# Kernel optimization log

Hardware: AMD Instinct MI355X
Metric: run time of the kernel (lower is better)

Reference implementation:

```python
import jax, jax.numpy as jnp
import numpy as np

# WGS84 constants
_A = 6378137.0
_E2 = 6.69437999014e-3  # first eccentricity squared

ALPHA = 1.0
GAMMA = 2.0
DYNAMIC_GAMMA = True
SCALE_FACTOR = 1.0


def _geodetic_to_ecef(lat_rad, lon_rad, h):
    sl, cl = jnp.sin(lat_rad), jnp.cos(lat_rad)
    so, co = jnp.sin(lon_rad), jnp.cos(lon_rad)
    N = _A / jnp.sqrt(1.0 - _E2 * sl * sl)
    x = (N + h) * cl * co
    y = (N + h) * cl * so
    z = (N * (1.0 - _E2) + h) * sl
    return jnp.stack([x, y, z], axis=-1)


def setup_inputs() -> dict:
    key = jax.random.key(0)
    k1, k2, k3, k4 = jax.random.split(key, 4)
    B = 4_000_000
    lat = jax.random.uniform(k1, (B,), jnp.float32, -80.0, 80.0)    # degrees
    lon = jax.random.uniform(k2, (B,), jnp.float32, -180.0, 180.0)  # degrees
    h = jax.random.uniform(k3, (B,), jnp.float32, 0.0, 1000.0)      # meters
    targets = jnp.stack([lat, lon, h], axis=1)
    ref_ecef = _geodetic_to_ecef(jnp.deg2rad(lat), jnp.deg2rad(lon), h)
    # predicted ECEF = true ECEF + ~meters of noise -> realistic GNSS error
    inputs = ref_ecef + 2.0 * jax.random.normal(k4, (B, 3), jnp.float32)
    return {"inputs": inputs, "targets": targets}


def _ecef_to_enu(pred_ecef, gt_geodetic):
    # Batched version of the per-sample ecef_to_enu_torch loop.
    lat = jnp.deg2rad(gt_geodetic[:, 0])
    lon = jnp.deg2rad(gt_geodetic[:, 1])
    h = gt_geodetic[:, 2]
    ref = _geodetic_to_ecef(lat, lon, h)
    d = pred_ecef - ref  # [B,3]
    sl, cl = jnp.sin(lat), jnp.cos(lat)
    so, co = jnp.sin(lon), jnp.cos(lon)
    dx, dy, dz = d[:, 0], d[:, 1], d[:, 2]
    e = -so * dx + co * dy
    n = -sl * co * dx - sl * so * dy + cl * dz
    u = cl * co * dx + cl * so * dy + sl * dz
    return jnp.stack([e, n, u], axis=1)  # [B,3]


def reference(inputs, targets):
    enu_errors = _ecef_to_enu(inputs, targets)                 # [B,3]
    squared_dist = jnp.sqrt(jnp.sum(enu_errors * enu_errors, axis=1))  # L2 norm [B]
    base_loss = squared_dist
    if DYNAMIC_GAMMA:
        dyn_gamma = GAMMA * jnp.exp(-SCALE_FACTOR * base_loss)
    else:
        dyn_gamma = GAMMA
    focal_weight = jnp.power(1.0 - jnp.sqrt(squared_dist / (jnp.max(squared_dist) + 1e-8)), dyn_gamma)
    focal_loss = ALPHA * focal_weight * base_loss
    return jnp.sqrt(jnp.mean(focal_loss * focal_loss))
```

## Files before the change

### kernel.cpp

```cpp
#include <hip/hip_runtime.h>
#include <math.h>


#define THREADS 256
#define PART_CAP 8192
#define BMAX_OFF 64
#define PART_OFF (64 + PART_CAP * 4)
#define DIST_OFF (1 << 20)

__device__ __forceinline__ void sincos8(const double* __restrict__ x,
                                        double* __restrict__ s,
                                        double* __restrict__ c) {
    const double TWO_OVER_PI = 0.636619772367581343076;
    const double PIO2_HI = 1.57079632679489655800e+00;
    const double PIO2_LO = 6.12323399573676603587e-17;

    double kd[8], r[8], r2[8];
    int q[8];
#pragma unroll
    for (int j = 0; j < 8; ++j) {
        kd[j] = rint(x[j] * TWO_OVER_PI);
        q[j] = ((int)kd[j]) & 3;
    }
#pragma unroll
    for (int j = 0; j < 8; ++j) {
        double rr = fma(-kd[j], PIO2_HI, x[j]);
        r[j] = fma(-kd[j], PIO2_LO, rr);
        r2[j] = r[j] * r[j];
    }
    double ps[8], pc[8];
#pragma unroll
    for (int j = 0; j < 8; ++j) { ps[j] = -2.50507602534068634195e-08;
                                  pc[j] =  2.08757232129817482790e-09; }
#pragma unroll
    for (int j = 0; j < 8; ++j) { ps[j] = fma(ps[j], r2[j],  2.75573137070700676789e-06);
                                  pc[j] = fma(pc[j], r2[j], -2.75573143513906633035e-07); }
#pragma unroll
    for (int j = 0; j < 8; ++j) { ps[j] = fma(ps[j], r2[j], -1.98412698298579493134e-04);
                                  pc[j] = fma(pc[j], r2[j],  2.48015872894767294178e-05); }
#pragma unroll
    for (int j = 0; j < 8; ++j) { ps[j] = fma(ps[j], r2[j],  8.33333333332248946124e-03);
                                  pc[j] = fma(pc[j], r2[j], -1.38888888888741095749e-03); }
#pragma unroll
    for (int j = 0; j < 8; ++j) { ps[j] = fma(ps[j], r2[j], -1.66666666666666324348e-01);
                                  pc[j] = fma(pc[j], r2[j],  4.16666666666666019037e-02); }
#pragma unroll
    for (int j = 0; j < 8; ++j) {
        double sv = fma(r2[j] * r[j], ps[j], r[j]);
        double cv = fma(r2[j] * r2[j], pc[j], fma(-0.5, r2[j], 1.0));
        double sr = (q[j] & 1) ? cv : sv;
        double cr = (q[j] & 1) ? sv : cv;
        s[j] = (q[j] & 2) ? -sr : sr;
        c[j] = ((q[j] + 1) & 2) ? -cr : cr;
    }
}

__device__ __forceinline__ void dist_group4(const float* __restrict__ lat,
                                            const float* __restrict__ lon,
                                            const float* __restrict__ hh,
                                            const float* __restrict__ px,
                                            const float* __restrict__ py,
                                            const float* __restrict__ pz,
                                            float* __restrict__ dout) {
    const float D2R = (float)0.017453292519943295;
    double x[8], s8[8], c8[8];
#pragma unroll
    for (int j = 0; j < 4; ++j) x[j] = (double)(lat[j] * D2R);
#pragma unroll
    for (int j = 0; j < 4; ++j) x[4 + j] = (double)(lon[j] * D2R);
    sincos8(x, s8, c8);

    const double A = 6378137.0, E2 = 0.00669437999014;
#pragma unroll
    for (int j = 0; j < 4; ++j) {
        double sl = s8[j], cl = c8[j], so = s8[4 + j], co = c8[4 + j];
        double h = (double)hh[j];
        double w = fma(-E2 * sl, sl, 1.0);
        double y = fma(-0.5, w, 1.5);
        y = y * fma(-0.5 * w, y * y, 1.5);
        y = y * fma(-0.5 * w, y * y, 1.5);
        double N = A * y, Nh = N + h;
        double X = Nh * cl * co;
        double Y = Nh * cl * so;
        double Z = fma(N, -E2, N + h) * sl;
        double dx = (double)px[j] - X;
        double dy = (double)py[j] - Y;
        double dz = (double)pz[j] - Z;
        dout[j] = sqrtf((float)(dx * dx + dy * dy + dz * dz));
    }
}

__device__ __forceinline__ float dist_one(float latd, float lond, float hf,
                                          float pxx, float pyy, float pzz) {
    float lat[4] = {latd, latd, latd, latd}, lon[4] = {lond, lond, lond, lond};
    float hh[4] = {hf, hf, hf, hf};
    float px[4] = {pxx, pxx, pxx, pxx}, py[4] = {pyy, pyy, pyy, pyy}, pz[4] = {pzz, pzz, pzz, pzz};
    float d[4];
    dist_group4(lat, lon, hh, px, py, pz, d);
    return d[0];
}

#define UNPACK4(ta, tb, tc, lat, lon, hh)                         \
    float lat[4] = {ta.x, ta.w, tb.z, tc.y};                      \
    float lon[4] = {ta.y, tb.x, tb.w, tc.z};                      \
    float hh[4]  = {ta.z, tb.y, tc.x, tc.w};

__global__ __launch_bounds__(THREADS, 3)
void k_pass1(const float* __restrict__ inp, const float* __restrict__ tgt,
             float* __restrict__ dist_arr, float* __restrict__ blockmax, long B) {
    long ngroups = (B + 3) >> 2;
    long nthreads = (long)gridDim.x * blockDim.x;
    long gstride = 2 * nthreads;
    float lmax = 0.0f;
    for (long g = (long)blockIdx.x * blockDim.x + threadIdx.x; g < ngroups; g += gstride) {
        long gA = g;
        long gB = g + nthreads;
        long baseA = gA << 2;
        long baseB = gB << 2;
        bool fastA = (baseA + 3 < B);
        bool fastB = (gB < ngroups) && (baseB + 3 < B);

        if (fastA && fastB) {
            const float4* tA = (const float4*)(tgt + 3 * baseA);
            const float4* pA = (const float4*)(inp + 3 * baseA);
            const float4* tB = (const float4*)(tgt + 3 * baseB);
            const float4* pB = (const float4*)(inp + 3 * baseB);
            float4 ta0 = tA[0], ta1 = tA[1], ta2 = tA[2];
            float4 pa0 = pA[0], pa1 = pA[1], pa2 = pA[2];
            float4 tb0 = tB[0], tb1 = tB[1], tb2 = tB[2];
            float4 pb0 = pB[0], pb1 = pB[1], pb2 = pB[2];

            UNPACK4(ta0, ta1, ta2, latA, lonA, hhA);
            UNPACK4(pa0, pa1, pa2, pxA, pyA, pzA);
            float dA[4];
            dist_group4(latA, lonA, hhA, pxA, pyA, pzA, dA);

            UNPACK4(tb0, tb1, tb2, latB, lonB, hhB);
            UNPACK4(pb0, pb1, pb2, pxB, pyB, pzB);
            float dB[4];
            dist_group4(latB, lonB, hhB, pxB, pyB, pzB, dB);

            if (dist_arr) {
                *(float4*)(dist_arr + baseA) = make_float4(dA[0], dA[1], dA[2], dA[3]);
                *(float4*)(dist_arr + baseB) = make_float4(dB[0], dB[1], dB[2], dB[3]);
            }
            lmax = fmaxf(lmax, fmaxf(fmaxf(dA[0], dA[1]), fmaxf(dA[2], dA[3])));
            lmax = fmaxf(lmax, fmaxf(fmaxf(dB[0], dB[1]), fmaxf(dB[2], dB[3])));
        } else {
            for (int pass = 0; pass < 2; ++pass) {
                long gg = pass ? gB : gA;
                if (gg >= ngroups) continue;
                long base = gg << 2;
                long end = base + 4 < B ? base + 4 : B;
                for (long i = base; i < end; ++i) {
                    float d = dist_one(tgt[3*i], tgt[3*i+1], tgt[3*i+2],
                                       inp[3*i], inp[3*i+1], inp[3*i+2]);
                    if (dist_arr) dist_arr[i] = d;
                    lmax = fmaxf(lmax, d);
                }
            }
        }
    }
    for (int off = 32; off > 0; off >>= 1)
        lmax = fmaxf(lmax, __shfl_down(lmax, off, 64));
    __shared__ float smax[THREADS / 64];
    if ((threadIdx.x & 63) == 0) smax[threadIdx.x >> 6] = lmax;
    __syncthreads();
    if (threadIdx.x == 0) {
        float m = smax[0];
        for (int w = 1; w < THREADS / 64; ++w) m = fmaxf(m, smax[w]);
        blockmax[blockIdx.x] = m;
    }
}

__device__ __forceinline__ double focal2(float d, float denom) {
    float g = 2.0f * __expf(-d);
    float b = 1.0f - sqrtf(d / denom);
    b = fmaxf(b, 0.0f);
    float wgt = __builtin_amdgcn_exp2f(g * __log2f(b));
    float fl = wgt * d;
    return (double)fl * (double)fl;
}

__global__ void k_pass2(const float* __restrict__ dist_arr,
                        const float* __restrict__ inp,
                        const float* __restrict__ tgt,
                        const float* __restrict__ blockmax, int nb1,
                        double* __restrict__ partials, long B) {
    __shared__ float smax[THREADS / 64];
    __shared__ double sacc[THREADS / 64];
    __shared__ float sb;
    int tid = threadIdx.x;

    float m = 0.0f;
    for (int i = tid; i < nb1; i += THREADS) m = fmaxf(m, blockmax[i]);
    for (int off = 32; off > 0; off >>= 1)
        m = fmaxf(m, __shfl_down(m, off, 64));
    if ((tid & 63) == 0) smax[tid >> 6] = m;
    __syncthreads();
    if (tid == 0) {
        float mm = smax[0];
        for (int w = 1; w < THREADS / 64; ++w) mm = fmaxf(mm, smax[w]);
        sb = mm;
    }
    __syncthreads();
    float denom = sb + 1e-8f;

    long ngroups = (B + 3) >> 2;
    long gstride = (long)gridDim.x * blockDim.x;
    double acc = 0.0;
    for (long g = (long)blockIdx.x * blockDim.x + tid; g < ngroups; g += gstride) {
        long base = g << 2;
        if (base + 3 < B) {
            float d0, d1, d2, d3;
            if (dist_arr) {
                float4 d4 = *(const float4*)(dist_arr + base);
                d0 = d4.x; d1 = d4.y; d2 = d4.z; d3 = d4.w;
            } else {
                const float4* t4 = (const float4*)(tgt + 3 * base);
                float4 ta = t4[0], tb = t4[1], tc = t4[2];
                const float4* p4 = (const float4*)(inp + 3 * base);
                float4 pa = p4[0], pb = p4[1], pc = p4[2];
                UNPACK4(ta, tb, tc, lat, lon, hh);
                UNPACK4(pa, pb, pc, px, py, pz);
                float d[4];
                dist_group4(lat, lon, hh, px, py, pz, d);
                d0 = d[0]; d1 = d[1]; d2 = d[2]; d3 = d[3];
            }
            acc += focal2(d0, denom) + focal2(d1, denom)
                 + focal2(d2, denom) + focal2(d3, denom);
        } else {
            for (long i = base; i < B; ++i) {
                float d = dist_arr ? dist_arr[i]
                                   : dist_one(tgt[3*i], tgt[3*i+1], tgt[3*i+2],
                                              inp[3*i], inp[3*i+1], inp[3*i+2]);
                acc += focal2(d, denom);
            }
        }
    }
    for (int off = 32; off > 0; off >>= 1)
        acc += __shfl_down(acc, off, 64);
    if ((tid & 63) == 0) sacc[tid >> 6] = acc;
    __syncthreads();
    if (tid == 0) {
        double s = sacc[0];
        for (int w = 1; w < THREADS / 64; ++w) s += sacc[w];
        partials[blockIdx.x] = s;
    }
}

__global__ void k_final(const double* __restrict__ partials, int nparts,
                        float* __restrict__ out, long B) {
    double acc = 0.0;
    for (int i = threadIdx.x; i < nparts; i += blockDim.x) acc += partials[i];
    for (int off = 32; off > 0; off >>= 1)
        acc += __shfl_down(acc, off, 64);
    __shared__ double lds[THREADS / 64];
    if ((threadIdx.x & 63) == 0) lds[threadIdx.x >> 6] = acc;
    __syncthreads();
    if (threadIdx.x == 0) {
        double s = lds[0];
        for (int w = 1; w < THREADS / 64; ++w) s += lds[w];
        out[0] = (float)sqrt(s / (double)B);
    }
}

extern "C" void kernel_launch(void* const* d_in, const int* in_sizes, int n_in,
                              void* d_out, int out_size, void* d_ws, size_t ws_size,
                              hipStream_t stream) {
    const float* inp = (const float*)d_in[0];
    const float* tgt = (const float*)d_in[1];
    float* out = (float*)d_out;
    long B = (long)in_sizes[0] / 3;

    float* blockmax = (float*)((char*)d_ws + BMAX_OFF);
    double* partials = (double*)((char*)d_ws + PART_OFF);
    float* dist_arr = nullptr;
    size_t need = (size_t)DIST_OFF + (size_t)B * sizeof(float);
    if (ws_size >= need) dist_arr = (float*)((char*)d_ws + DIST_OFF);

    long ngroups = (B + 3) >> 2;

    long nhalf = (ngroups + 1) >> 1;
    int nb1 = (int)((nhalf + THREADS - 1) / THREADS);
    if (nb1 > PART_CAP) nb1 = PART_CAP;
    if (nb1 < 1) nb1 = 1;

    int nb2 = (int)((ngroups + THREADS - 1) / THREADS);
    if (nb2 > PART_CAP) nb2 = PART_CAP;
    if (nb2 < 1) nb2 = 1;

    k_pass1<<<nb1, THREADS, 0, stream>>>(inp, tgt, dist_arr, blockmax, B);
    k_pass2<<<nb2, THREADS, 0, stream>>>(dist_arr, inp, tgt, blockmax, nb1, partials, B);
    k_final<<<1, THREADS, 0, stream>>>(partials, nb2, out, B);
}
```

Measured before the change: 132.3 us.

## Store intermediate distances as fp16 and fold final reduction into pass2 via ticket

The per-sample distance buffer written by pass1 and read by pass2 is now stored as half precision, halving that intermediate traffic. The separate final-reduction kernel is removed: the last pass2 block, found through an atomic ticket counter, sums the partials and writes the output. The fp16 rounding of distances (values in the several-metre range) adds relative error to the focal loss and the max-normalised weight. The ticket is reset by every pass1 block, which is fine only because pass1 completes before pass2 on the stream.

```diff
diff --git a/kernel.cpp b/kernel.cpp
--- a/kernel.cpp
+++ b/kernel.cpp
@@ -1,9 +1,11 @@
 #include <hip/hip_runtime.h>
+#include <hip/hip_fp16.h>
 #include <math.h>
 
 
 #define THREADS 256
 #define PART_CAP 8192
+#define TICKET_OFF 0
 #define BMAX_OFF 64
 #define PART_OFF (64 + PART_CAP * 4)
 #define DIST_OFF (1 << 20)
@@ -105,9 +107,18 @@
     float lon[4] = {ta.y, tb.x, tb.w, tc.z};                      \
     float hh[4]  = {ta.z, tb.y, tc.x, tc.w};
 
+__device__ __forceinline__ void store_half4(__half* p, float d0, float d1, float d2, float d3) {
+    union { __half2 h2[2]; uint2 u; } pk;
+    pk.h2[0] = __floats2half2_rn(d0, d1);
+    pk.h2[1] = __floats2half2_rn(d2, d3);
+    *(uint2*)p = pk.u;
+}
+
 __global__ __launch_bounds__(THREADS, 3)
 void k_pass1(const float* __restrict__ inp, const float* __restrict__ tgt,
-             float* __restrict__ dist_arr, float* __restrict__ blockmax, long B) {
+             __half* __restrict__ dist_arr, float* __restrict__ blockmax,
+             unsigned* __restrict__ ticket, long B) {
+    if (threadIdx.x == 0) *ticket = 0u;
     long ngroups = (B + 3) >> 2;
     long nthreads = (long)gridDim.x * blockDim.x;
     long gstride = 2 * nthreads;
@@ -141,8 +152,8 @@
             dist_group4(latB, lonB, hhB, pxB, pyB, pzB, dB);
 
             if (dist_arr) {
-                *(float4*)(dist_arr + baseA) = make_float4(dA[0], dA[1], dA[2], dA[3]);
-                *(float4*)(dist_arr + baseB) = make_float4(dB[0], dB[1], dB[2], dB[3]);
+                store_half4(dist_arr + baseA, dA[0], dA[1], dA[2], dA[3]);
+                store_half4(dist_arr + baseB, dB[0], dB[1], dB[2], dB[3]);
             }
             lmax = fmaxf(lmax, fmaxf(fmaxf(dA[0], dA[1]), fmaxf(dA[2], dA[3])));
             lmax = fmaxf(lmax, fmaxf(fmaxf(dB[0], dB[1]), fmaxf(dB[2], dB[3])));
@@ -155,7 +166,7 @@
                 for (long i = base; i < end; ++i) {
                     float d = dist_one(tgt[3*i], tgt[3*i+1], tgt[3*i+2],
                                        inp[3*i], inp[3*i+1], inp[3*i+2]);
-                    if (dist_arr) dist_arr[i] = d;
+                    if (dist_arr) dist_arr[i] = __float2half_rn(d);
                     lmax = fmaxf(lmax, d);
                 }
             }
@@ -182,14 +193,17 @@
     return (double)fl * (double)fl;
 }
 
-__global__ void k_pass2(const float* __restrict__ dist_arr,
+__global__ void k_pass2(const __half* __restrict__ dist_arr,
                         const float* __restrict__ inp,
                         const float* __restrict__ tgt,
                         const float* __restrict__ blockmax, int nb1,
-                        double* __restrict__ partials, long B) {
+                        double* __restrict__ partials,
+                        unsigned* __restrict__ ticket,
+                        float* __restrict__ out, long B) {
     __shared__ float smax[THREADS / 64];
     __shared__ double sacc[THREADS / 64];
     __shared__ float sb;
+    __shared__ unsigned stick;
     int tid = threadIdx.x;
 
     float m = 0.0f;
@@ -214,8 +228,11 @@
         if (base + 3 < B) {
             float d0, d1, d2, d3;
             if (dist_arr) {
-                float4 d4 = *(const float4*)(dist_arr + base);
-                d0 = d4.x; d1 = d4.y; d2 = d4.z; d3 = d4.w;
+                union { uint2 u; __half2 h2[2]; } pk;
+                pk.u = *(const uint2*)(dist_arr + base);
+                float2 lo = __half22float2(pk.h2[0]);
+                float2 hi = __half22float2(pk.h2[1]);
+                d0 = lo.x; d1 = lo.y; d2 = hi.x; d3 = hi.y;
             } else {
                 const float4* t4 = (const float4*)(tgt + 3 * base);
                 float4 ta = t4[0], tb = t4[1], tc = t4[2];
@@ -231,7 +248,7 @@
                  + focal2(d2, denom) + focal2(d3, denom);
         } else {
             for (long i = base; i < B; ++i) {
-                float d = dist_arr ? dist_arr[i]
+                float d = dist_arr ? __half2float(dist_arr[i])
                                    : dist_one(tgt[3*i], tgt[3*i+1], tgt[3*i+2],
                                               inp[3*i], inp[3*i+1], inp[3*i+2]);
                 acc += focal2(d, denom);
@@ -246,22 +263,24 @@
         double s = sacc[0];
         for (int w = 1; w < THREADS / 64; ++w) s += sacc[w];
         partials[blockIdx.x] = s;
-    }
-}
-
-__global__ void k_final(const double* __restrict__ partials, int nparts,
-                        float* __restrict__ out, long B) {
-    double acc = 0.0;
-    for (int i = threadIdx.x; i < nparts; i += blockDim.x) acc += partials[i];
-    for (int off = 32; off > 0; off >>= 1)
-        acc += __shfl_down(acc, off, 64);
-    __shared__ double lds[THREADS / 64];
-    if ((threadIdx.x & 63) == 0) lds[threadIdx.x >> 6] = acc;
-    __syncthreads();
-    if (threadIdx.x == 0) {
-        double s = lds[0];
-        for (int w = 1; w < THREADS / 64; ++w) s += lds[w];
-        out[0] = (float)sqrt(s / (double)B);
+        __threadfence();
+        stick = atomicAdd(ticket, 1u);
+    }
+    __syncthreads();
+
+    if (stick == gridDim.x - 1) {
+        __threadfence();
+        double a = 0.0;
+        for (int i = tid; i < (int)gridDim.x; i += THREADS) a += partials[i];
+        for (int off = 32; off > 0; off >>= 1)
+            a += __shfl_down(a, off, 64);
+        if ((tid & 63) == 0) sacc[tid >> 6] = a;
+        __syncthreads();
+        if (tid == 0) {
+            double s = sacc[0];
+            for (int w = 1; w < THREADS / 64; ++w) s += sacc[w];
+            out[0] = (float)sqrt(s / (double)B);
+        }
     }
 }
 
@@ -273,11 +292,12 @@
     float* out = (float*)d_out;
     long B = (long)in_sizes[0] / 3;
 
+    unsigned* ticket = (unsigned*)((char*)d_ws + TICKET_OFF);
     float* blockmax = (float*)((char*)d_ws + BMAX_OFF);
     double* partials = (double*)((char*)d_ws + PART_OFF);
-    float* dist_arr = nullptr;
-    size_t need = (size_t)DIST_OFF + (size_t)B * sizeof(float);
-    if (ws_size >= need) dist_arr = (float*)((char*)d_ws + DIST_OFF);
+    __half* dist_arr = nullptr;
+    size_t need = (size_t)DIST_OFF + (size_t)B * sizeof(__half);
+    if (ws_size >= need) dist_arr = (__half*)((char*)d_ws + DIST_OFF);
 
     long ngroups = (B + 3) >> 2;
 
@@ -290,7 +310,7 @@
     if (nb2 > PART_CAP) nb2 = PART_CAP;
     if (nb2 < 1) nb2 = 1;
 
-    k_pass1<<<nb1, THREADS, 0, stream>>>(inp, tgt, dist_arr, blockmax, B);
-    k_pass2<<<nb2, THREADS, 0, stream>>>(dist_arr, inp, tgt, blockmax, nb1, partials, B);
-    k_final<<<1, THREADS, 0, stream>>>(partials, nb2, out, B);
-}
+    k_pass1<<<nb1, THREADS, 0, stream>>>(inp, tgt, dist_arr, blockmax, ticket, B);
+    k_pass2<<<nb2, THREADS, 0, stream>>>(dist_arr, inp, tgt, blockmax, nb1,
+                                         partials, ticket, out, B);
+}
```

Result: slower. 234.3 us (+77.1%).
